# Kernel optimization log

Hardware: AMD Instinct MI355X
Metric: run time of the kernel (lower is better)

## Reference

```python
import jax, jax.numpy as jnp
import numpy as np

EPS = 1e-5  # torch InstanceNorm1d default eps

def _inst_norm(x, gamma, beta):
    # x: [B,S,D]; torch InstanceNorm1d normalizes over seq axis per channel (biased var)
    mu = x.mean(axis=1, keepdims=True)
    var = x.var(axis=1, keepdims=True)
    return (x - mu) / jnp.sqrt(var + EPS) * gamma + beta

def _encoder_layer(x, neg_dist, log_scale, Wq, Wk, Wv, alpha, g1, b1, W1, bW1, W2, bW2, g2, b2):
    q = x @ Wq.T
    k = x @ Wk.T
    v = x @ Wv.T
    s = log_scale * alpha * neg_dist            # [B,S,S]
    es = jnp.exp(s)
    ek = jnp.exp(k)                             # [B,S,D]
    num = es @ (ek * v)                         # [B,S,D]
    den = es @ ek                               # [B,S,D]
    weighted = jnp.nan_to_num(num) / jnp.nan_to_num(den)
    aft = jax.nn.sigmoid(q) * weighted
    h = _inst_norm(x + aft, g1, b1)
    ff = jax.nn.relu(h @ W1.T + bW1) @ W2.T + bW2
    return _inst_norm(h + ff, g2, b2)

def setup_inputs() -> dict:
    key = jax.random.key(0)
    B, N, D, F, L = 32, 999, 128, 512, 6
    ks = jax.random.split(key, 32)
    n = lambda i, shape, s: (jax.random.normal(ks[i], shape, dtype=jnp.float32) * s)
    inp = {
        "depot_xy": jax.random.uniform(ks[0], (B, 1, 2), dtype=jnp.float32),
        "node_xy_demand": jax.random.uniform(ks[1], (B, N, 3), dtype=jnp.float32),
        "dist": jax.random.uniform(ks[2], (B, N + 1, N + 1), dtype=jnp.float32),
        "log_scale": jnp.ones((1,), dtype=jnp.float32),
        "flag": jax.random.randint(ks[3], (B,), 0, 2, dtype=jnp.int32),
        # embedding params
        "Wd": n(4, (D, 2), 0.1), "bd": jnp.zeros((D,), jnp.float32),
        "Wn": n(5, (D, 3), 0.1), "bn": jnp.zeros((D,), jnp.float32),
        "Win": n(6, (D, D), 0.05), "bin_": jnp.zeros((D,), jnp.float32),
        "Wout": n(7, (D, D), 0.05), "bout": jnp.zeros((D,), jnp.float32),
        # stacked per-layer params
        "Wq": n(8, (L, D, D), 0.05), "Wk": n(9, (L, D, D), 0.05), "Wv": n(10, (L, D, D), 0.05),
        "alpha": jnp.ones((L,), jnp.float32),
        "g1": jnp.ones((L, D), jnp.float32), "b1": jnp.zeros((L, D), jnp.float32),
        "W1": n(11, (L, F, D), 0.05), "bW1": jnp.zeros((L, F), jnp.float32),
        "W2": n(12, (L, D, F), 0.05), "bW2": jnp.zeros((L, D), jnp.float32),
        "g2": jnp.ones((L, D), jnp.float32), "b2": jnp.zeros((L, D), jnp.float32),
    }
    return inp

def reference(depot_xy, node_xy_demand, dist, log_scale, flag,
              Wd, bd, Wn, bn, Win, bin_, Wout, bout,
              Wq, Wk, Wv, alpha, g1, b1, W1, bW1, W2, bW2, g2, b2):
    B, N, _ = node_xy_demand.shape
    ed = depot_xy @ Wd.T + bd                    # [B,1,D]
    en = node_xy_demand @ Wn.T + bn              # [B,N,D]
    en = en.at[:, 0, :].set(en[:, 0, :] @ Win.T + bin_)
    out = jnp.concatenate([ed, en], axis=1)      # [B,N+1,D]
    idx = ((1 - flag) * N).astype(jnp.int32)     # index 0 or N per batch
    rows = jnp.arange(B)
    last = out[rows, idx] @ Wout.T + bout        # [B,D]
    out = out.at[rows, idx].set(last)
    neg_dist = -dist
    for i in range(Wq.shape[0]):
        out = _encoder_layer(out, neg_dist, log_scale,
                             Wq[i], Wk[i], Wv[i], alpha[i],
                             g1[i], b1[i], W1[i], bW1[i], W2[i], bW2[i], g2[i], b2[i])
    return out
```

## Files before the change

### kernel.cpp

```cpp
#include <hip/hip_runtime.h>
#include <hip/hip_bf16.h>
#include <float.h>
#include <math.h>

#define B 32
#define NN 999
#define S 1000
#define D 128
#define F 512
#define L 6
#define EPSN 1e-5f
#define WSTR 180224

typedef __attribute__((ext_vector_type(4))) float f32x4;
typedef __attribute__((ext_vector_type(4))) short s16x4;
typedef __attribute__((ext_vector_type(8))) short s16x8;

#if defined(__has_builtin)
#if __has_builtin(__builtin_amdgcn_mfma_f32_16x16x16bf16_1k)
#define HAVE_MFMA16 1
#endif
#if __has_builtin(__builtin_amdgcn_mfma_f32_16x16x32_bf16)
#define HAVE_MFMA32 1
#endif
#endif

#ifdef HAVE_MFMA16
#define MFMA16(a, b, c) __builtin_amdgcn_mfma_f32_16x16x16bf16_1k((a), (b), (c), 0, 0, 0)
#else
static __device__ __forceinline__ f32x4 mfma16_asm(s16x4 a, s16x4 b, f32x4 c) {
    asm volatile("v_mfma_f32_16x16x16_bf16 %0, %1, %2, %0\n\ts_nop 7\n\ts_nop 7"
                 : "+v"(c) : "v"(a), "v"(b));
    return c;
}
#define MFMA16(a, b, c) mfma16_asm((a), (b), (c))
#endif

#ifdef HAVE_MFMA32
#define MFMA32(a, b, c) __builtin_amdgcn_mfma_f32_16x16x32_bf16((a), (b), (c), 0, 0, 0)
#else
static __device__ __forceinline__ f32x4 mfma32_asm(s16x8 a, s16x8 b, f32x4 c) {
    asm volatile("v_mfma_f32_16x16x32_bf16 %0, %1, %2, %0\n\ts_nop 7\n\ts_nop 7"
                 : "+v"(c) : "v"(a), "v"(b));
    return c;
}
#define MFMA32(a, b, c) mfma32_asm((a), (b), (c))
#endif

__device__ __forceinline__ float n2n(float v) {
    if (v != v) return 0.f;
    if (isinf(v)) return v > 0.f ? FLT_MAX : -FLT_MAX;
    return v;
}

__device__ __forceinline__ unsigned short f2bf(float x) {
    unsigned u = __float_as_uint(x);
    return (unsigned short)((u + 0x7fffu + ((u >> 16) & 1u)) >> 16);
}

__device__ __forceinline__ float bf2f(unsigned short v) {
    return __uint_as_float(((unsigned)v) << 16);
}

__global__ __launch_bounds__(256) void k_wprep(
        const float* __restrict__ Wq, const float* __restrict__ Wk,
        const float* __restrict__ Wv, const float* __restrict__ W1,
        const float* __restrict__ W2, unsigned short* __restrict__ wbf) {
    int bx = blockIdx.x, l = blockIdx.y;
    const float* src; int doff, off;
    if (bx < 8)       { src = Wq + (size_t)l * 16384; doff = 0;      off = bx * 2048; }
    else if (bx < 16) { src = Wk + (size_t)l * 16384; doff = 16384;  off = (bx - 8) * 2048; }
    else if (bx < 24) { src = Wv + (size_t)l * 16384; doff = 32768;  off = (bx - 16) * 2048; }
    else if (bx < 56) { src = W1 + (size_t)l * 65536; doff = 49152;  off = (bx - 24) * 2048; }
    else              { src = W2 + (size_t)l * 65536; doff = 114688; off = (bx - 56) * 2048; }
    int i = off + threadIdx.x * 8;
    float4 a4 = *(const float4*)(src + i);
    float4 b4 = *(const float4*)(src + i + 4);
    s16x8 p = {(short)f2bf(a4.x), (short)f2bf(a4.y), (short)f2bf(a4.z), (short)f2bf(a4.w),
               (short)f2bf(b4.x), (short)f2bf(b4.y), (short)f2bf(b4.z), (short)f2bf(b4.w)};
    *(s16x8*)(wbf + (size_t)l * WSTR + doff + i) = p;
}

__global__ __launch_bounds__(256) void k_prep(
        const float* __restrict__ dist, unsigned short* __restrict__ nd) {
    int row = blockIdx.x;
    int col = threadIdx.x * 4;
    unsigned short* op = nd + (size_t)row * 1024 + col;
    if (col < 1000) {
        float4 v = *(const float4*)(dist + (size_t)row * 1000 + col);
        s16x4 p = {(short)f2bf(v.x), (short)f2bf(v.y), (short)f2bf(v.z), (short)f2bf(v.w)};
        *(s16x4*)op = p;
    } else {
        s16x4 z = {0, 0, 0, 0};
        *(s16x4*)op = z;
    }
}

__global__ __launch_bounds__(128) void k_embed(
        const float* __restrict__ depot, const float* __restrict__ node,
        const float* __restrict__ Wd, const float* __restrict__ bd,
        const float* __restrict__ Wn, const float* __restrict__ bn,
        float* __restrict__ x) {
    int row = blockIdx.x;
    int b = row / S, s = row % S;
    int d = threadIdx.x;
    float o;
    if (s == 0) {
        float x0 = depot[b * 2 + 0], x1 = depot[b * 2 + 1];
        o = Wd[d * 2 + 0] * x0 + Wd[d * 2 + 1] * x1 + bd[d];
    } else {
        const float* p = node + ((size_t)b * NN + (s - 1)) * 3;
        o = Wn[d * 3 + 0] * p[0] + Wn[d * 3 + 1] * p[1] + Wn[d * 3 + 2] * p[2] + bn[d];
    }
    x[(size_t)row * D + d] = o;
}

__global__ __launch_bounds__(128) void k_rowxform(
        float* __restrict__ x, const float* __restrict__ W,
        const float* __restrict__ bias, const int* __restrict__ flag, int mode) {
    int b = blockIdx.x;
    int d = threadIdx.x;
    __shared__ float row[D];
    int r = (mode == 0) ? 1 : (1 - flag[b]) * NN;
    float* xr = x + ((size_t)b * S + r) * D;
    row[d] = xr[d];
    __syncthreads();
    float acc = bias[d];
    for (int e = 0; e < D; e += 4) {
        const float4 w = *(const float4*)(W + (size_t)d * D + e);
        acc += w.x * row[e] + w.y * row[e + 1] + w.z * row[e + 2] + w.w * row[e + 3];
    }
    xr[d] = acc;
}

__global__ __launch_bounds__(256) void k_qkv(
        const float* __restrict__ yprev, const float* __restrict__ part2, int hasnorm,
        const float* __restrict__ gp, const float* __restrict__ bp,
        const unsigned short* __restrict__ wl,
        unsigned short* __restrict__ sqb, unsigned short* __restrict__ mT) {
    int blk = blockIdx.x;
    int b = blk >> 4, rb = blk & 15;
    int s0 = rb * 64;
    int tid = threadIdx.x, lane = tid & 63, wid = tid >> 6;
    __shared__ __align__(16) unsigned short lds[18432];
    __shared__ float nsc[128], nsh[128];
    __shared__ float accv[256];
    unsigned short* xs = lds;
    unsigned short* wt0 = lds + 2560;

    if (hasnorm) {
        int st = tid >> 7, d = tid & 127;
        float s = 0.f;
#pragma unroll
        for (int c = 0; c < 16; c++) s += part2[(size_t)(b * 32 + c * 2 + st) * 128 + d];
        accv[tid] = s;
    }
    __syncthreads();
    if (tid < 128) {
        float scv = 1.f, shv = 0.f;
        if (hasnorm) {
            float mu = accv[tid] * (1.f / S);
            float var = accv[128 + tid] * (1.f / S) - mu * mu;
            float rs = rsqrtf(var + EPSN);
            scv = rs * gp[tid];
            shv = bp[tid] - mu * scv;
        }
        nsc[tid] = scv; nsh[tid] = shv;
    }
    __syncthreads();

    f32x4 acc[3][8];
#pragma unroll
    for (int mm = 0; mm < 3; mm++)
#pragma unroll
        for (int cf = 0; cf < 8; cf++) acc[mm][cf] = {0.f, 0.f, 0.f, 0.f};

    for (int k0 = 0; k0 < D; k0 += 32) {
        {
            int i = tid >> 2, kq = (tid & 3) * 8;
            int s = s0 + i;
            int gs = s < S ? s : S - 1;
            const float* gpx = yprev + ((size_t)b * S + gs) * D + k0 + kq;
            float4 a4 = *(const float4*)gpx;
            float4 b4 = *(const float4*)(gpx + 4);
            const float* scp = &nsc[k0 + kq];
            const float* shp = &nsh[k0 + kq];
            s16x4 p0 = {(short)f2bf(a4.x * scp[0] + shp[0]), (short)f2bf(a4.y * scp[1] + shp[1]),
                        (short)f2bf(a4.z * scp[2] + shp[2]), (short)f2bf(a4.w * scp[3] + shp[3])};
            s16x4 p1 = {(short)f2bf(b4.x * scp[4] + shp[4]), (short)f2bf(b4.y * scp[5] + shp[5]),
                        (short)f2bf(b4.z * scp[6] + shp[6]), (short)f2bf(b4.w * scp[7] + shp[7])};
            *(s16x4*)&xs[i * 40 + kq] = p0;
            *(s16x4*)&xs[i * 40 + kq + 4] = p1;
        }
#pragma unroll
        for (int u0 = 0; u0 < 6; u0++) {
            int u = tid + u0 * 256;
            int mm = u >> 9;
            int v = u & 511;
            int c = v >> 2, kq = (v & 3) * 8;
            s16x8 w = *(const s16x8*)(wl + (size_t)mm * 16384 + (size_t)c * D + k0 + kq);
            *(s16x8*)&wt0[mm * 5120 + c * 40 + kq] = w;
        }
        __syncthreads();
#pragma unroll
        for (int ks = 0; ks < 2; ks++) {
            int ko = ks * 16 + (lane >> 4) * 4;
            s16x4 a = *(const s16x4*)&xs[(wid * 16 + (lane & 15)) * 40 + ko];
#pragma unroll
            for (int mm = 0; mm < 3; mm++)
#pragma unroll
                for (int cf = 0; cf < 8; cf++) {
                    s16x4 bf = *(const s16x4*)&wt0[mm * 5120 + (cf * 16 + (lane & 15)) * 40 + ko];
                    acc[mm][cf] = MFMA16(a, bf, acc[mm][cf]);
                }
        }
        __syncthreads();
    }

    unsigned short* tile = lds;
    int sl0 = wid * 16 + (lane >> 4) * 4;
#pragma unroll
    for (int cf = 0; cf < 8; cf++) {
        int d = cf * 16 + (lane & 15);
        s16x4 p0, p1;
#pragma unroll
        for (int r = 0; r < 4; r++) {
            int s = s0 + sl0 + r;
            if (s < S) {
                float qv = acc[0][cf][r], kv = acc[1][cf][r], vv = acc[2][cf][r];
                float ek = __expf(kv);
                sqb[((size_t)b * S + s) * D + d] = f2bf(1.f / (1.f + __expf(-qv)));
                p0[r] = (short)f2bf(ek * vv);
                p1[r] = (short)f2bf(ek);
            } else { p0[r] = 0; p1[r] = 0; }
        }
        *(s16x4*)&tile[d * 72 + sl0] = p0;
        *(s16x4*)&tile[(d + 128) * 72 + sl0] = p1;
    }
    __syncthreads();
    {
        unsigned short* base = mT + (((size_t)b * 16 + rb) * 256) * 64;
#pragma unroll
        for (int j = 0; j < 8; j++) {
            int u = j * 256 + tid;
            int d = u >> 3, sp = u & 7;
            int o = sp ^ (d & 7);
            s16x8 v = *(const s16x8*)&tile[d * 72 + o * 8];
            *(s16x8*)(base + (size_t)u * 8) = v;
        }
    }
}

__global__ __launch_bounds__(512, 2) void k_attn(
        const float* __restrict__ yprev, const float* __restrict__ part2, int hasnorm,
        const float* __restrict__ gp, const float* __restrict__ bp,
        const unsigned short* __restrict__ sqb,
        const unsigned short* __restrict__ mT, const unsigned short* __restrict__ nd,
        const float* __restrict__ log_scale, const float* __restrict__ alpha, int l,
        float* __restrict__ y, float* __restrict__ part) {
    int blk0 = blockIdx.x;
    int blk = (blk0 & 7) * 64 + (blk0 >> 3);
    int b = blk >> 4, ib = blk & 15;
    int i0 = ib * 64;
    int tid = threadIdx.x, lane = tid & 63, wid = tid >> 6;
    int wr = wid & 3, wh = wid >> 2;
    __shared__ __align__(16) unsigned short esL[64 * 64];
    __shared__ __align__(16) unsigned short mtL[256 * 64];
    __shared__ float accvA[256];
    float sc = log_scale[0] * alpha[l];

    if (hasnorm && tid < 256) {
        int st = tid >> 7, d = tid & 127;
        float s = 0.f;
#pragma unroll
        for (int c = 0; c < 16; c++) s += part2[(size_t)(b * 32 + c * 2 + st) * 128 + d];
        accvA[tid] = s;
    }
    __syncthreads();

    float rsc[8], rsh[8];
#pragma unroll
    for (int cf = 0; cf < 8; cf++) {
        int d = cf * 16 + (lane & 15);
        float scv = 1.f, shv = 0.f;
        if (hasnorm) {
            float mu = accvA[d] * (1.f / S);
            float var = accvA[128 + d] * (1.f / S) - mu * mu;
            float rs = rsqrtf(var + EPSN);
            scv = rs * gp[d];
            shv = bp[d] - mu * scv;
        }
        rsc[cf] = scv; rsh[cf] = shv;
    }

    f32x4 acc[8];
#pragma unroll
    for (int cf = 0; cf < 8; cf++) acc[cf] = {0.f, 0.f, 0.f, 0.f};

    int erow = tid >> 3, og = tid & 7;
    int gi = i0 + erow; if (gi > 999) gi = 999;
    const unsigned short* ndr = nd + (size_t)b * 1000 * 1024 + (size_t)gi * 1024 + og * 8;
    const unsigned short* mtb = mT + (size_t)b * 16 * 16384;
    unsigned short* esw = &esL[erow * 64 + ((og ^ (erow & 7)) * 8)];

    s16x8 cn = *(const s16x8*)(ndr);
    s16x8 cm[4];
#pragma unroll
    for (int j = 0; j < 4; j++)
        cm[j] = *(const s16x8*)(mtb + (size_t)(j * 512 + tid) * 8);

    for (int kc = 0; kc < 16; kc++) {
        s16x8 o0;
#pragma unroll
        for (int j = 0; j < 8; j++)
            o0[j] = (short)f2bf(__expf(-sc * bf2f((unsigned short)cn[j])));
        int kn = kc < 15 ? kc + 1 : 15;
        cn = *(const s16x8*)(ndr + kn * 64);
        __syncthreads();
        *(s16x8*)esw = o0;
#pragma unroll
        for (int j = 0; j < 4; j++)
            *(s16x8*)&mtL[(j * 512 + tid) * 8] = cm[j];
#pragma unroll
        for (int j = 0; j < 4; j++)
            cm[j] = *(const s16x8*)(mtb + (size_t)kn * 16384 + (size_t)(j * 512 + tid) * 8);
        __syncthreads();
#pragma unroll
        for (int ks = 0; ks < 2; ks++) {
            int arow = wr * 16 + (lane & 15);
            int ag = ks * 4 + (lane >> 4);
            s16x8 a = *(const s16x8*)&esL[arow * 64 + ((ag ^ (arow & 7)) * 8)];
            __builtin_amdgcn_s_setprio(1);
#pragma unroll
            for (int cf = 0; cf < 8; cf++) {
                int c = cf * 16 + wh * 128 + (lane & 15);
                s16x8 bf = *(const s16x8*)&mtL[c * 64 + ((ag ^ (c & 7)) * 8)];
                acc[cf] = MFMA32(a, bf, acc[cf]);
            }
            __builtin_amdgcn_s_setprio(0);
        }
    }

    __syncthreads();
    float* pw = (float*)mtL;
    if (wh == 1) {
#pragma unroll
        for (int cf = 0; cf < 8; cf++) {
            int c = cf * 16 + (lane & 15);
#pragma unroll
            for (int r = 0; r < 4; r++) {
                int rl = wr * 16 + (lane >> 4) * 4 + r;
                pw[rl * 128 + c] = acc[cf][r];
            }
        }
    }
    __syncthreads();
    float* sw = (float*)esL;
    if (wh == 0) {
#pragma unroll
        for (int cf = 0; cf < 8; cf++) {
            int d = cf * 16 + (lane & 15);
            float s = 0.f, s2 = 0.f;
#pragma unroll
            for (int r = 0; r < 4; r++) {
                int rl = wr * 16 + (lane >> 4) * 4 + r;
                int i = i0 + rl;
                if (i < S) {
                    size_t off = ((size_t)b * S + i) * D + d;
                    float w = n2n(acc[cf][r]) / n2n(pw[rl * 128 + d]);
                    float xv = yprev[off] * rsc[cf] + rsh[cf];
                    float yv = xv + bf2f(sqb[off]) * w;
                    y[off] = yv;
                    s += yv;
                    s2 = fmaf(yv, yv, s2);
                }
            }
            s += __shfl_xor(s, 16); s += __shfl_xor(s, 32);
            s2 += __shfl_xor(s2, 16); s2 += __shfl_xor(s2, 32);
            if (lane < 16) {
                sw[(wr * 2 + 0) * 128 + d] = s;
                sw[(wr * 2 + 1) * 128 + d] = s2;
            }
        }
    }
    __syncthreads();
    if (tid < 256) {
        int st = tid >> 7, d = tid & 127;
        float v = sw[(0 * 2 + st) * 128 + d] + sw[(1 * 2 + st) * 128 + d] +
                  sw[(2 * 2 + st) * 128 + d] + sw[(3 * 2 + st) * 128 + d];
        part[((size_t)(b * 16 + ib) * 2 + st) * 128 + d] = v;
    }
}

__global__ __launch_bounds__(256) void k_ffn(
        const float* __restrict__ ya, const float* __restrict__ part1,
        const float* __restrict__ gp, const float* __restrict__ bp,
        const unsigned short* __restrict__ w1b, const unsigned short* __restrict__ w2b,
        const float* __restrict__ bW1, const float* __restrict__ bW2,
        float* __restrict__ yb, float* __restrict__ part) {
    int blk = blockIdx.x;
    int b = blk >> 4, rb = blk & 15;
    int r0 = rb * 64;
    int tid = threadIdx.x, lane = tid & 63, wid = tid >> 6;
    __shared__ __align__(16) unsigned short hs[64 * 128];
    __shared__ __align__(16) unsigned short w1c[64 * 128];
    __shared__ __align__(16) unsigned short tc[64 * 72];
    __shared__ __align__(16) unsigned short w2c[128 * 64];
    __shared__ float nsc[128], nsh[128];
    __shared__ float accv[256];

    {
        int st = tid >> 7, d = tid & 127;
        float s = 0.f;
#pragma unroll
        for (int c = 0; c < 16; c++) s += part1[(size_t)(b * 32 + c * 2 + st) * 128 + d];
        accv[tid] = s;
    }
    __syncthreads();
    if (tid < 128) {
        float mu = accv[tid] * (1.f / S);
        float var = accv[128 + tid] * (1.f / S) - mu * mu;
        float rs = rsqrtf(var + EPSN);
        float scv = rs * gp[tid];
        nsc[tid] = scv;
        nsh[tid] = bp[tid] - mu * scv;
    }
    __syncthreads();

    {
        int i = tid >> 2;
        int gs = r0 + i; if (gs >= S) gs = S - 1;
        const float* gpx = ya + ((size_t)b * S + gs) * D;
#pragma unroll
        for (int q = 0; q < 4; q++) {
            int col = (tid & 3) * 32 + q * 8;
            int g = col >> 3;
            float4 a4 = *(const float4*)(gpx + col);
            float4 b4 = *(const float4*)(gpx + col + 4);
            const float* scp = &nsc[col];
            const float* shp = &nsh[col];
            s16x4 p0 = {(short)f2bf(a4.x * scp[0] + shp[0]), (short)f2bf(a4.y * scp[1] + shp[1]),
                        (short)f2bf(a4.z * scp[2] + shp[2]), (short)f2bf(a4.w * scp[3] + shp[3])};
            s16x4 p1 = {(short)f2bf(b4.x * scp[4] + shp[4]), (short)f2bf(b4.y * scp[5] + shp[5]),
                        (short)f2bf(b4.z * scp[6] + shp[6]), (short)f2bf(b4.w * scp[7] + shp[7])};
            int base = i * 128 + ((g ^ (i & 7)) * 8);
            *(s16x4*)&hs[base] = p0;
            *(s16x4*)&hs[base + 4] = p1;
        }
    }

    f32x4 yacc[8];
#pragma unroll
    for (int cf = 0; cf < 8; cf++) yacc[cf] = {0.f, 0.f, 0.f, 0.f};

    for (int fc = 0; fc < 8; fc++) {
        int c0 = fc * 64;
        {
            int f = tid >> 2;
#pragma unroll
            for (int q = 0; q < 4; q++) {
                int col = (tid & 3) * 32 + q * 8;
                int g = col >> 3;
                s16x8 w = *(const s16x8*)(w1b + (size_t)(c0 + f) * D + col);
                *(s16x8*)&w1c[f * 128 + ((g ^ (f & 7)) * 8)] = w;
            }
        }
        {
            int d2 = tid >> 1;
#pragma unroll
            for (int q = 0; q < 4; q++) {
                int g = (tid & 1) * 4 + q;
                s16x8 w = *(const s16x8*)(w2b + (size_t)d2 * F + c0 + g * 8);
                *(s16x8*)&w2c[d2 * 64 + ((g ^ (d2 & 7)) * 8)] = w;
            }
        }
        __syncthreads();
        f32x4 tacc[4];
#pragma unroll
        for (int c4 = 0; c4 < 4; c4++) tacc[c4] = {0.f, 0.f, 0.f, 0.f};
#pragma unroll
        for (int ks = 0; ks < 4; ks++) {
            int g = ks * 4 + (lane >> 4);
            int arow = wid * 16 + (lane & 15);
            s16x8 a = *(const s16x8*)&hs[arow * 128 + ((g ^ (arow & 7)) * 8)];
#pragma unroll
            for (int c4 = 0; c4 < 4; c4++) {
                int brow = c4 * 16 + (lane & 15);
                s16x8 bf = *(const s16x8*)&w1c[brow * 128 + ((g ^ (brow & 7)) * 8)];
                tacc[c4] = MFMA32(a, bf, tacc[c4]);
            }
        }
#pragma unroll
        for (int c4 = 0; c4 < 4; c4++) {
            int col = c4 * 16 + (lane & 15);
            float bias = bW1[c0 + col];
#pragma unroll
            for (int r = 0; r < 4; r++) {
                int rl = wid * 16 + (lane >> 4) * 4 + r;
                tc[rl * 72 + col] = f2bf(fmaxf(tacc[c4][r] + bias, 0.f));
            }
        }
        __syncthreads();
#pragma unroll
        for (int ks = 0; ks < 2; ks++) {
            int ko = ks * 32 + (lane >> 4) * 8;
            int g = ks * 4 + (lane >> 4);
            s16x8 a = *(const s16x8*)&tc[(wid * 16 + (lane & 15)) * 72 + ko];
#pragma unroll
            for (int cf = 0; cf < 8; cf++) {
                int brow = cf * 16 + (lane & 15);
                s16x8 bf = *(const s16x8*)&w2c[brow * 64 + ((g ^ (brow & 7)) * 8)];
                yacc[cf] = MFMA32(a, bf, yacc[cf]);
            }
        }
        __syncthreads();
    }

    float* pw = (float*)w1c;
#pragma unroll
    for (int cf = 0; cf < 8; cf++) {
        int d = cf * 16 + (lane & 15);
        float bias = bW2[d];
        float s = 0.f, s2 = 0.f;
#pragma unroll
        for (int r = 0; r < 4; r++) {
            int rl = wid * 16 + (lane >> 4) * 4 + r;
            int row = r0 + rl;
            if (row < S) {
                float hval = bf2f(hs[rl * 128 + (((d >> 3) ^ (rl & 7)) * 8) + (d & 7)]);
                float yv = hval + yacc[cf][r] + bias;
                yb[((size_t)b * S + row) * D + d] = yv;
                s += yv;
                s2 = fmaf(yv, yv, s2);
            }
        }
        s += __shfl_xor(s, 16); s += __shfl_xor(s, 32);
        s2 += __shfl_xor(s2, 16); s2 += __shfl_xor(s2, 32);
        if (lane < 16) {
            pw[(wid * 2 + 0) * 128 + d] = s;
            pw[(wid * 2 + 1) * 128 + d] = s2;
        }
    }
    __syncthreads();
    {
        int st = tid >> 7, d = tid & 127;
        float v = pw[(0 * 2 + st) * 128 + d] + pw[(1 * 2 + st) * 128 + d] +
                  pw[(2 * 2 + st) * 128 + d] + pw[(3 * 2 + st) * 128 + d];
        part[((size_t)(b * 16 + rb) * 2 + st) * 128 + d] = v;
    }
}

__global__ __launch_bounds__(256) void k_finalize(
        const float* __restrict__ part, float* __restrict__ acc) {
    int i = blockIdx.x * 256 + threadIdx.x;
    int b = i >> 8, k = i & 255;
    float s = 0.f;
#pragma unroll
    for (int c = 0; c < 16; c++) s += part[(size_t)(b * 16 + c) * 256 + k];
    acc[i] = s;
}

__global__ __launch_bounds__(256) void k_norm(
        const float* __restrict__ y, const float* __restrict__ acc,
        const float* __restrict__ g, const float* __restrict__ bb,
        float* __restrict__ out) {
    size_t i = (size_t)blockIdx.x * 256 + threadIdx.x;
    int d = (int)(i % D);
    int b = (int)(i / ((size_t)S * D));
    float mu = acc[b * 256 + d] * (1.f / S);
    float var = acc[b * 256 + 128 + d] * (1.f / S) - mu * mu;
    float v = (y[i] - mu) * rsqrtf(var + EPSN);
    out[i] = v * g[d] + bb[d];
}

extern "C" void kernel_launch(void* const* d_in, const int* in_sizes, int n_in,
                              void* d_out, int out_size, void* d_ws, size_t ws_size,
                              hipStream_t stream) {
    const float* depot = (const float*)d_in[0];
    const float* node  = (const float*)d_in[1];
    const float* dist  = (const float*)d_in[2];
    const float* log_scale = (const float*)d_in[3];
    const int*   flag  = (const int*)d_in[4];
    const float* Wd   = (const float*)d_in[5];
    const float* bd   = (const float*)d_in[6];
    const float* Wn   = (const float*)d_in[7];
    const float* bn   = (const float*)d_in[8];
    const float* Win  = (const float*)d_in[9];
    const float* bin_ = (const float*)d_in[10];
    const float* Wout = (const float*)d_in[11];
    const float* bout = (const float*)d_in[12];
    const float* Wq   = (const float*)d_in[13];
    const float* Wk   = (const float*)d_in[14];
    const float* Wv   = (const float*)d_in[15];
    const float* alpha= (const float*)d_in[16];
    const float* g1   = (const float*)d_in[17];
    const float* b1   = (const float*)d_in[18];
    const float* W1   = (const float*)d_in[19];
    const float* bW1  = (const float*)d_in[20];
    const float* W2   = (const float*)d_in[21];
    const float* bW2  = (const float*)d_in[22];
    const float* g2   = (const float*)d_in[23];
    const float* b2   = (const float*)d_in[24];

    float* ws = (float*)d_ws;
    size_t nxd = (size_t)B * S * D;
    float* ya    = ws;
    float* yb    = ws + nxd;
    float* part1 = ws + 2 * nxd;
    float* part2 = part1 + 131072;
    float* accb2 = part2 + 131072;
    unsigned short* sqb = (unsigned short*)(accb2 + 8192);
    unsigned short* mT  = sqb + nxd;
    unsigned short* wbf = mT + (size_t)B * 16 * 256 * 64;
    unsigned short* nd  = wbf + (size_t)L * WSTR;

    k_wprep<<<dim3(88, 6), 256, 0, stream>>>(Wq, Wk, Wv, W1, W2, wbf);
    k_prep<<<B * S, 256, 0, stream>>>(dist, nd);
    k_embed<<<B * S, 128, 0, stream>>>(depot, node, Wd, bd, Wn, bn, yb);
    k_rowxform<<<B, 128, 0, stream>>>(yb, Win, bin_, flag, 0);
    k_rowxform<<<B, 128, 0, stream>>>(yb, Wout, bout, flag, 1);

    for (int l = 0; l < L; l++) {
        int hasnorm = (l > 0) ? 1 : 0;
        const float* gpn = g2 + (l > 0 ? (l - 1) : 0) * D;
        const float* bpn = b2 + (l > 0 ? (l - 1) : 0) * D;
        const unsigned short* wl = wbf + (size_t)l * WSTR;
        k_qkv<<<B * 16, 256, 0, stream>>>(yb, part2, hasnorm, gpn, bpn, wl, sqb, mT);
        k_attn<<<B * 16, 512, 0, stream>>>(yb, part2, hasnorm, gpn, bpn,
                                           sqb, mT, nd, log_scale, alpha, l, ya, part1);
        k_ffn<<<B * 16, 256, 0, stream>>>(ya, part1, g1 + l * D, b1 + l * D,
                                          wl + 49152, wl + 114688,
                                          bW1 + (size_t)l * F, bW2 + (size_t)l * D, yb, part2);
    }
    k_finalize<<<32, 256, 0, stream>>>(part2, accb2);
    k_norm<<<B * S * D / 256, 256, 0, stream>>>(yb, accb2, g2 + 5 * D, b2 + 5 * D, (float*)d_out);
}
```

Measured before the change: 643.0 us.

## Read MFMA weight operands directly from global memory instead of staging in LDS

In the QKV and FFN kernels, weight fragments are now loaded straight from global memory (L2/L1-cached) into registers for each MFMA instead of being cooperatively staged into shared memory per K-chunk. The QKV kernel also stages the whole normalized input row tile once with an XOR swizzle and switches from 16x16x16 to 16x16x32 bf16 MFMA. This removes per-chunk barriers and LDS traffic and lowers LDS usage, which may raise occupancy. The cost is more redundant global/cache reads of weights across waves, with load latency that is no longer hidden behind barriers. The FFN epilogue scratch is moved onto the remaining tc buffer.

```diff
diff --git a/kernel.cpp b/kernel.cpp
--- a/kernel.cpp
+++ b/kernel.cpp
@@ -146,7 +146,6 @@
     __shared__ float nsc[128], nsh[128];
     __shared__ float accv[256];
     unsigned short* xs = lds;
-    unsigned short* wt0 = lds + 2560;
 
     if (hasnorm) {
         int st = tid >> 7, d = tid & 127;
@@ -169,53 +168,50 @@
     }
     __syncthreads();
 
-    f32x4 acc[3][8];
-#pragma unroll
-    for (int mm = 0; mm < 3; mm++)
-#pragma unroll
-        for (int cf = 0; cf < 8; cf++) acc[mm][cf] = {0.f, 0.f, 0.f, 0.f};
-
-    for (int k0 = 0; k0 < D; k0 += 32) {
-        {
-            int i = tid >> 2, kq = (tid & 3) * 8;
-            int s = s0 + i;
-            int gs = s < S ? s : S - 1;
-            const float* gpx = yprev + ((size_t)b * S + gs) * D + k0 + kq;
-            float4 a4 = *(const float4*)gpx;
-            float4 b4 = *(const float4*)(gpx + 4);
-            const float* scp = &nsc[k0 + kq];
-            const float* shp = &nsh[k0 + kq];
+    {
+        int i = tid >> 2;
+        int s = s0 + i; int gs = s < S ? s : S - 1;
+        const float* gpx = yprev + ((size_t)b * S + gs) * D;
+#pragma unroll
+        for (int q = 0; q < 4; q++) {
+            int col = (tid & 3) * 32 + q * 8;
+            int g = col >> 3;
+            float4 a4 = *(const float4*)(gpx + col);
+            float4 b4 = *(const float4*)(gpx + col + 4);
+            const float* scp = &nsc[col];
+            const float* shp = &nsh[col];
             s16x4 p0 = {(short)f2bf(a4.x * scp[0] + shp[0]), (short)f2bf(a4.y * scp[1] + shp[1]),
                         (short)f2bf(a4.z * scp[2] + shp[2]), (short)f2bf(a4.w * scp[3] + shp[3])};
             s16x4 p1 = {(short)f2bf(b4.x * scp[4] + shp[4]), (short)f2bf(b4.y * scp[5] + shp[5]),
                         (short)f2bf(b4.z * scp[6] + shp[6]), (short)f2bf(b4.w * scp[7] + shp[7])};
-            *(s16x4*)&xs[i * 40 + kq] = p0;
-            *(s16x4*)&xs[i * 40 + kq + 4] = p1;
-        }
-#pragma unroll
-        for (int u0 = 0; u0 < 6; u0++) {
-            int u = tid + u0 * 256;
-            int mm = u >> 9;
-            int v = u & 511;
-            int c = v >> 2, kq = (v & 3) * 8;
-            s16x8 w = *(const s16x8*)(wl + (size_t)mm * 16384 + (size_t)c * D + k0 + kq);
-            *(s16x8*)&wt0[mm * 5120 + c * 40 + kq] = w;
-        }
-        __syncthreads();
-#pragma unroll
-        for (int ks = 0; ks < 2; ks++) {
-            int ko = ks * 16 + (lane >> 4) * 4;
-            s16x4 a = *(const s16x4*)&xs[(wid * 16 + (lane & 15)) * 40 + ko];
-#pragma unroll
-            for (int mm = 0; mm < 3; mm++)
-#pragma unroll
-                for (int cf = 0; cf < 8; cf++) {
-                    s16x4 bf = *(const s16x4*)&wt0[mm * 5120 + (cf * 16 + (lane & 15)) * 40 + ko];
-                    acc[mm][cf] = MFMA16(a, bf, acc[mm][cf]);
-                }
-        }
-        __syncthreads();
-    }
+            int base = i * 128 + ((g ^ (i & 7)) * 8);
+            *(s16x4*)&xs[base] = p0;
+            *(s16x4*)&xs[base + 4] = p1;
+        }
+    }
+    __syncthreads();
+
+    f32x4 acc[3][8];
+#pragma unroll
+    for (int mm = 0; mm < 3; mm++)
+#pragma unroll
+        for (int cf = 0; cf < 8; cf++) acc[mm][cf] = {0.f, 0.f, 0.f, 0.f};
+
+    int arow = wid * 16 + (lane & 15);
+    int klo = (lane >> 4) * 8;
+    for (int ks = 0; ks < 4; ks++) {
+        int g = ks * 4 + (lane >> 4);
+        s16x8 a = *(const s16x8*)&xs[arow * 128 + ((g ^ (arow & 7)) * 8)];
+#pragma unroll
+        for (int mm = 0; mm < 3; mm++)
+#pragma unroll
+            for (int cf = 0; cf < 8; cf++) {
+                int wrow = cf * 16 + (lane & 15);
+                s16x8 bf = *(const s16x8*)(wl + (size_t)mm * 16384 + (size_t)wrow * D + ks * 32 + klo);
+                acc[mm][cf] = MFMA32(a, bf, acc[mm][cf]);
+            }
+    }
+    __syncthreads();
 
     unsigned short* tile = lds;
     int sl0 = wid * 16 + (lane >> 4) * 4;
@@ -403,9 +399,7 @@
     int r0 = rb * 64;
     int tid = threadIdx.x, lane = tid & 63, wid = tid >> 6;
     __shared__ __align__(16) unsigned short hs[64 * 128];
-    __shared__ __align__(16) unsigned short w1c[64 * 128];
     __shared__ __align__(16) unsigned short tc[64 * 72];
-    __shared__ __align__(16) unsigned short w2c[128 * 64];
     __shared__ float nsc[128], nsh[128];
     __shared__ float accv[256];
 
@@ -448,45 +442,27 @@
             *(s16x4*)&hs[base + 4] = p1;
         }
     }
+    __syncthreads();
 
     f32x4 yacc[8];
 #pragma unroll
     for (int cf = 0; cf < 8; cf++) yacc[cf] = {0.f, 0.f, 0.f, 0.f};
 
+    int klo = (lane >> 4) * 8;
+    int arow = wid * 16 + (lane & 15);
     for (int fc = 0; fc < 8; fc++) {
         int c0 = fc * 64;
-        {
-            int f = tid >> 2;
-#pragma unroll
-            for (int q = 0; q < 4; q++) {
-                int col = (tid & 3) * 32 + q * 8;
-                int g = col >> 3;
-                s16x8 w = *(const s16x8*)(w1b + (size_t)(c0 + f) * D + col);
-                *(s16x8*)&w1c[f * 128 + ((g ^ (f & 7)) * 8)] = w;
-            }
-        }
-        {
-            int d2 = tid >> 1;
-#pragma unroll
-            for (int q = 0; q < 4; q++) {
-                int g = (tid & 1) * 4 + q;
-                s16x8 w = *(const s16x8*)(w2b + (size_t)d2 * F + c0 + g * 8);
-                *(s16x8*)&w2c[d2 * 64 + ((g ^ (d2 & 7)) * 8)] = w;
-            }
-        }
-        __syncthreads();
         f32x4 tacc[4];
 #pragma unroll
         for (int c4 = 0; c4 < 4; c4++) tacc[c4] = {0.f, 0.f, 0.f, 0.f};
 #pragma unroll
         for (int ks = 0; ks < 4; ks++) {
             int g = ks * 4 + (lane >> 4);
-            int arow = wid * 16 + (lane & 15);
             s16x8 a = *(const s16x8*)&hs[arow * 128 + ((g ^ (arow & 7)) * 8)];
 #pragma unroll
             for (int c4 = 0; c4 < 4; c4++) {
-                int brow = c4 * 16 + (lane & 15);
-                s16x8 bf = *(const s16x8*)&w1c[brow * 128 + ((g ^ (brow & 7)) * 8)];
+                int wrow = c0 + c4 * 16 + (lane & 15);
+                s16x8 bf = *(const s16x8*)(w1b + (size_t)wrow * D + ks * 32 + klo);
                 tacc[c4] = MFMA32(a, bf, tacc[c4]);
             }
         }
@@ -503,20 +479,19 @@
         __syncthreads();
 #pragma unroll
         for (int ks = 0; ks < 2; ks++) {
-            int ko = ks * 32 + (lane >> 4) * 8;
-            int g = ks * 4 + (lane >> 4);
+            int ko = ks * 32 + klo;
             s16x8 a = *(const s16x8*)&tc[(wid * 16 + (lane & 15)) * 72 + ko];
 #pragma unroll
             for (int cf = 0; cf < 8; cf++) {
-                int brow = cf * 16 + (lane & 15);
-                s16x8 bf = *(const s16x8*)&w2c[brow * 64 + ((g ^ (brow & 7)) * 8)];
+                int wrow = cf * 16 + (lane & 15);
+                s16x8 bf = *(const s16x8*)(w2b + (size_t)wrow * F + c0 + ko);
                 yacc[cf] = MFMA32(a, bf, yacc[cf]);
             }
         }
         __syncthreads();
     }
 
-    float* pw = (float*)w1c;
+    float* pw = (float*)tc;
 #pragma unroll
     for (int cf = 0; cf < 8; cf++) {
         int d = cf * 16 + (lane & 15);
```

Measured after the change: 1.014 ms. 1.58x slower.

## Double attention row tile per block to reuse staged mT across 128 rows

Applied to the files above, without the earlier changes.

Each attention block now covers 128 query rows instead of 64, with two accumulator sets per wave, so every staged chunk of the exp(k)/exp(k)*v matrix in LDS feeds twice as many MFMAs. The grid shrinks from 512 to 256 blocks, halving global reloads of mT. The epilogue runs in two passes, and the FFN partial-sum reader is updated to read 8 partials per batch. The cost is more registers for the accumulators and only 256 blocks, which may leave the GPU's compute units underused.

```diff
diff --git a/kernel.cpp b/kernel.cpp
--- a/kernel.cpp
+++ b/kernel.cpp
@@ -259,12 +259,12 @@
         const float* __restrict__ log_scale, const float* __restrict__ alpha, int l,
         float* __restrict__ y, float* __restrict__ part) {
     int blk0 = blockIdx.x;
-    int blk = (blk0 & 7) * 64 + (blk0 >> 3);
-    int b = blk >> 4, ib = blk & 15;
-    int i0 = ib * 64;
+    int blk = (blk0 & 7) * 32 + (blk0 >> 3);
+    int b = blk >> 3, ib = blk & 7;
+    int i0 = ib * 128;
     int tid = threadIdx.x, lane = tid & 63, wid = tid >> 6;
     int wr = wid & 3, wh = wid >> 2;
-    __shared__ __align__(16) unsigned short esL[64 * 64];
+    __shared__ __align__(16) unsigned short esL[128 * 64];
     __shared__ __align__(16) unsigned short mtL[256 * 64];
     __shared__ float accvA[256];
     float sc = log_scale[0] * alpha[l];
@@ -293,31 +293,40 @@
         rsc[cf] = scv; rsh[cf] = shv;
     }
 
-    f32x4 acc[8];
-#pragma unroll
-    for (int cf = 0; cf < 8; cf++) acc[cf] = {0.f, 0.f, 0.f, 0.f};
-
-    int erow = tid >> 3, og = tid & 7;
+    f32x4 acc[2][8];
+#pragma unroll
+    for (int rf = 0; rf < 2; rf++)
+#pragma unroll
+        for (int cf = 0; cf < 8; cf++) acc[rf][cf] = {0.f, 0.f, 0.f, 0.f};
+
+    int erow = tid >> 2;
     int gi = i0 + erow; if (gi > 999) gi = 999;
-    const unsigned short* ndr = nd + (size_t)b * 1000 * 1024 + (size_t)gi * 1024 + og * 8;
+    const unsigned short* ndr = nd + (size_t)b * 1000 * 1024 + (size_t)gi * 1024 + (tid & 3) * 16;
     const unsigned short* mtb = mT + (size_t)b * 16 * 16384;
-    unsigned short* esw = &esL[erow * 64 + ((og ^ (erow & 7)) * 8)];
-
-    s16x8 cn = *(const s16x8*)(ndr);
+    int eg = (tid & 3) * 2;
+    unsigned short* esw0 = &esL[erow * 64 + ((eg ^ (erow & 7)) * 8)];
+    unsigned short* esw1 = &esL[erow * 64 + (((eg + 1) ^ (erow & 7)) * 8)];
+
+    s16x8 cnA = *(const s16x8*)(ndr);
+    s16x8 cnB = *(const s16x8*)(ndr + 8);
     s16x8 cm[4];
 #pragma unroll
     for (int j = 0; j < 4; j++)
         cm[j] = *(const s16x8*)(mtb + (size_t)(j * 512 + tid) * 8);
 
     for (int kc = 0; kc < 16; kc++) {
-        s16x8 o0;
-#pragma unroll
-        for (int j = 0; j < 8; j++)
-            o0[j] = (short)f2bf(__expf(-sc * bf2f((unsigned short)cn[j])));
+        s16x8 o0, o1;
+#pragma unroll
+        for (int j = 0; j < 8; j++) {
+            o0[j] = (short)f2bf(__expf(-sc * bf2f((unsigned short)cnA[j])));
+            o1[j] = (short)f2bf(__expf(-sc * bf2f((unsigned short)cnB[j])));
+        }
         int kn = kc < 15 ? kc + 1 : 15;
-        cn = *(const s16x8*)(ndr + kn * 64);
-        __syncthreads();
-        *(s16x8*)esw = o0;
+        cnA = *(const s16x8*)(ndr + kn * 64);
+        cnB = *(const s16x8*)(ndr + kn * 64 + 8);
+        __syncthreads();
+        *(s16x8*)esw0 = o0;
+        *(s16x8*)esw1 = o1;
 #pragma unroll
         for (int j = 0; j < 4; j++)
             *(s16x8*)&mtL[(j * 512 + tid) * 8] = cm[j];
@@ -327,30 +336,60 @@
         __syncthreads();
 #pragma unroll
         for (int ks = 0; ks < 2; ks++) {
-            int arow = wr * 16 + (lane & 15);
             int ag = ks * 4 + (lane >> 4);
-            s16x8 a = *(const s16x8*)&esL[arow * 64 + ((ag ^ (arow & 7)) * 8)];
+            int arow0 = wr * 32 + (lane & 15);
+            int arow1 = arow0 + 16;
+            s16x8 a0 = *(const s16x8*)&esL[arow0 * 64 + ((ag ^ (arow0 & 7)) * 8)];
+            s16x8 a1 = *(const s16x8*)&esL[arow1 * 64 + ((ag ^ (arow1 & 7)) * 8)];
             __builtin_amdgcn_s_setprio(1);
 #pragma unroll
             for (int cf = 0; cf < 8; cf++) {
                 int c = cf * 16 + wh * 128 + (lane & 15);
                 s16x8 bf = *(const s16x8*)&mtL[c * 64 + ((ag ^ (c & 7)) * 8)];
-                acc[cf] = MFMA32(a, bf, acc[cf]);
+                acc[0][cf] = MFMA32(a0, bf, acc[0][cf]);
+                acc[1][cf] = MFMA32(a1, bf, acc[1][cf]);
             }
             __builtin_amdgcn_s_setprio(0);
         }
     }
 
-    __syncthreads();
+    float sacc[8], s2acc[8];
+#pragma unroll
+    for (int cf = 0; cf < 8; cf++) { sacc[cf] = 0.f; s2acc[cf] = 0.f; }
     float* pw = (float*)mtL;
-    if (wh == 1) {
-#pragma unroll
-        for (int cf = 0; cf < 8; cf++) {
-            int c = cf * 16 + (lane & 15);
-#pragma unroll
-            for (int r = 0; r < 4; r++) {
-                int rl = wr * 16 + (lane >> 4) * 4 + r;
-                pw[rl * 128 + c] = acc[cf][r];
+#pragma unroll
+    for (int rf = 0; rf < 2; rf++) {
+        __syncthreads();
+        if (wh == 1) {
+#pragma unroll
+            for (int cf = 0; cf < 8; cf++) {
+                int c = cf * 16 + (lane & 15);
+#pragma unroll
+                for (int r = 0; r < 4; r++) {
+                    int lrow = wr * 16 + (lane >> 4) * 4 + r;
+                    pw[lrow * 128 + c] = acc[rf][cf][r];
+                }
+            }
+        }
+        __syncthreads();
+        if (wh == 0) {
+#pragma unroll
+            for (int cf = 0; cf < 8; cf++) {
+                int d = cf * 16 + (lane & 15);
+#pragma unroll
+                for (int r = 0; r < 4; r++) {
+                    int lrow = wr * 16 + (lane >> 4) * 4 + r;
+                    int i = i0 + wr * 32 + rf * 16 + (lane >> 4) * 4 + r;
+                    if (i < S) {
+                        size_t off = ((size_t)b * S + i) * D + d;
+                        float w = n2n(acc[rf][cf][r]) / n2n(pw[lrow * 128 + d]);
+                        float xv = yprev[off] * rsc[cf] + rsh[cf];
+                        float yv = xv + bf2f(sqb[off]) * w;
+                        y[off] = yv;
+                        sacc[cf] += yv;
+                        s2acc[cf] = fmaf(yv, yv, s2acc[cf]);
+                    }
+                }
             }
         }
     }
@@ -360,21 +399,7 @@
 #pragma unroll
         for (int cf = 0; cf < 8; cf++) {
             int d = cf * 16 + (lane & 15);
-            float s = 0.f, s2 = 0.f;
-#pragma unroll
-            for (int r = 0; r < 4; r++) {
-                int rl = wr * 16 + (lane >> 4) * 4 + r;
-                int i = i0 + rl;
-                if (i < S) {
-                    size_t off = ((size_t)b * S + i) * D + d;
-                    float w = n2n(acc[cf][r]) / n2n(pw[rl * 128 + d]);
-                    float xv = yprev[off] * rsc[cf] + rsh[cf];
-                    float yv = xv + bf2f(sqb[off]) * w;
-                    y[off] = yv;
-                    s += yv;
-                    s2 = fmaf(yv, yv, s2);
-                }
-            }
+            float s = sacc[cf], s2 = s2acc[cf];
             s += __shfl_xor(s, 16); s += __shfl_xor(s, 32);
             s2 += __shfl_xor(s2, 16); s2 += __shfl_xor(s2, 32);
             if (lane < 16) {
@@ -388,7 +413,7 @@
         int st = tid >> 7, d = tid & 127;
         float v = sw[(0 * 2 + st) * 128 + d] + sw[(1 * 2 + st) * 128 + d] +
                   sw[(2 * 2 + st) * 128 + d] + sw[(3 * 2 + st) * 128 + d];
-        part[((size_t)(b * 16 + ib) * 2 + st) * 128 + d] = v;
+        part[((size_t)(b * 8 + ib) * 2 + st) * 128 + d] = v;
     }
 }
 
@@ -413,7 +438,7 @@
         int st = tid >> 7, d = tid & 127;
         float s = 0.f;
 #pragma unroll
-        for (int c = 0; c < 16; c++) s += part1[(size_t)(b * 32 + c * 2 + st) * 128 + d];
+        for (int c = 0; c < 8; c++) s += part1[(size_t)(b * 8 + c) * 256 + st * 128 + d];
         accv[tid] = s;
     }
     __syncthreads();
@@ -626,8 +651,8 @@
         const float* bpn = b2 + (l > 0 ? (l - 1) : 0) * D;
         const unsigned short* wl = wbf + (size_t)l * WSTR;
         k_qkv<<<B * 16, 256, 0, stream>>>(yb, part2, hasnorm, gpn, bpn, wl, sqb, mT);
-        k_attn<<<B * 16, 512, 0, stream>>>(yb, part2, hasnorm, gpn, bpn,
-                                           sqb, mT, nd, log_scale, alpha, l, ya, part1);
+        k_attn<<<B * 8, 512, 0, stream>>>(yb, part2, hasnorm, gpn, bpn,
+                                          sqb, mT, nd, log_scale, alpha, l, ya, part1);
         k_ffn<<<B * 16, 256, 0, stream>>>(ya, part1, g1 + l * D, b1 + l * D,
                                           wl + 49152, wl + 114688,
                                           bW1 + (size_t)l * F, bW2 + (size_t)l * D, yb, part2);
```

New measurement: 699.0 us. +8.7%, slower.

## Double-buffer LDS tiles in attention kernel to cut per-iteration barriers

Applied to the files above, without the earlier changes.

Converts the es/mT shared-memory staging in k_attn to a two-slot ping-pong buffer. The next chunk is written into the alternate slot while MFMAs read the current one, so each iteration needs one barrier instead of two. Global loads are issued two chunks ahead. LDS use roughly doubles (about 80KB per block), which may limit occupancy below the two blocks per CU requested by launch_bounds. accvA is aliased into esL to save space.

```diff
diff --git a/kernel.cpp b/kernel.cpp
--- a/kernel.cpp
+++ b/kernel.cpp
@@ -264,11 +264,11 @@
     int i0 = ib * 64;
     int tid = threadIdx.x, lane = tid & 63, wid = tid >> 6;
     int wr = wid & 3, wh = wid >> 2;
-    __shared__ __align__(16) unsigned short esL[64 * 64];
-    __shared__ __align__(16) unsigned short mtL[256 * 64];
-    __shared__ float accvA[256];
+    __shared__ __align__(16) unsigned short esL[2][64 * 64];
+    __shared__ __align__(16) unsigned short mtL[2][256 * 64];
     float sc = log_scale[0] * alpha[l];
 
+    float* accvA = (float*)esL;
     if (hasnorm && tid < 256) {
         int st = tid >> 7, d = tid & 127;
         float s = 0.f;
@@ -292,6 +292,7 @@
         }
         rsc[cf] = scv; rsh[cf] = shv;
     }
+    __syncthreads();
 
     f32x4 acc[8];
 #pragma unroll
@@ -301,48 +302,65 @@
     int gi = i0 + erow; if (gi > 999) gi = 999;
     const unsigned short* ndr = nd + (size_t)b * 1000 * 1024 + (size_t)gi * 1024 + og * 8;
     const unsigned short* mtb = mT + (size_t)b * 16 * 16384;
-    unsigned short* esw = &esL[erow * 64 + ((og ^ (erow & 7)) * 8)];
+    int esoff = erow * 64 + ((og ^ (erow & 7)) * 8);
 
     s16x8 cn = *(const s16x8*)(ndr);
     s16x8 cm[4];
 #pragma unroll
     for (int j = 0; j < 4; j++)
         cm[j] = *(const s16x8*)(mtb + (size_t)(j * 512 + tid) * 8);
-
-    for (int kc = 0; kc < 16; kc++) {
+    {
         s16x8 o0;
 #pragma unroll
         for (int j = 0; j < 8; j++)
             o0[j] = (short)f2bf(__expf(-sc * bf2f((unsigned short)cn[j])));
-        int kn = kc < 15 ? kc + 1 : 15;
-        cn = *(const s16x8*)(ndr + kn * 64);
-        __syncthreads();
-        *(s16x8*)esw = o0;
+        *(s16x8*)&esL[0][esoff] = o0;
 #pragma unroll
         for (int j = 0; j < 4; j++)
-            *(s16x8*)&mtL[(j * 512 + tid) * 8] = cm[j];
-#pragma unroll
-        for (int j = 0; j < 4; j++)
-            cm[j] = *(const s16x8*)(mtb + (size_t)kn * 16384 + (size_t)(j * 512 + tid) * 8);
-        __syncthreads();
+            *(s16x8*)&mtL[0][(j * 512 + tid) * 8] = cm[j];
+    }
+    cn = *(const s16x8*)(ndr + 64);
+#pragma unroll
+    for (int j = 0; j < 4; j++)
+        cm[j] = *(const s16x8*)(mtb + (size_t)16384 + (size_t)(j * 512 + tid) * 8);
+    __syncthreads();
+
+    int cur = 0;
+    for (int kc = 0; kc < 16; kc++) {
+        if (kc < 15) {
+            s16x8 o0;
+#pragma unroll
+            for (int j = 0; j < 8; j++)
+                o0[j] = (short)f2bf(__expf(-sc * bf2f((unsigned short)cn[j])));
+            *(s16x8*)&esL[cur ^ 1][esoff] = o0;
+#pragma unroll
+            for (int j = 0; j < 4; j++)
+                *(s16x8*)&mtL[cur ^ 1][(j * 512 + tid) * 8] = cm[j];
+            int kn = (kc + 2 <= 15) ? kc + 2 : 15;
+            cn = *(const s16x8*)(ndr + kn * 64);
+#pragma unroll
+            for (int j = 0; j < 4; j++)
+                cm[j] = *(const s16x8*)(mtb + (size_t)kn * 16384 + (size_t)(j * 512 + tid) * 8);
+        }
 #pragma unroll
         for (int ks = 0; ks < 2; ks++) {
             int arow = wr * 16 + (lane & 15);
             int ag = ks * 4 + (lane >> 4);
-            s16x8 a = *(const s16x8*)&esL[arow * 64 + ((ag ^ (arow & 7)) * 8)];
+            s16x8 a = *(const s16x8*)&esL[cur][arow * 64 + ((ag ^ (arow & 7)) * 8)];
             __builtin_amdgcn_s_setprio(1);
 #pragma unroll
             for (int cf = 0; cf < 8; cf++) {
                 int c = cf * 16 + wh * 128 + (lane & 15);
-                s16x8 bf = *(const s16x8*)&mtL[c * 64 + ((ag ^ (c & 7)) * 8)];
+                s16x8 bf = *(const s16x8*)&mtL[cur][c * 64 + ((ag ^ (c & 7)) * 8)];
                 acc[cf] = MFMA32(a, bf, acc[cf]);
             }
             __builtin_amdgcn_s_setprio(0);
         }
-    }
-
-    __syncthreads();
-    float* pw = (float*)mtL;
+        __syncthreads();
+        cur ^= 1;
+    }
+
+    float* pw = (float*)mtL[0];
     if (wh == 1) {
 #pragma unroll
         for (int cf = 0; cf < 8; cf++) {
```

Measured after the change: 645.5 us. About the same (+0.4%).
